# Optimization experiments

Measured on AMD Instinct MI355X. Metric: run time of the kernel, lower is better.

## Reference

```python
import jax, jax.numpy as jnp
import numpy as np

HIDDEN = 2048
HEADS = 32
GROUPS = 8
HEAD_DIM = HIDDEN // HEADS  # 64
BSZ = 1
SEQ = 2048
KV_DIM = GROUPS * HEAD_DIM  # 512


def setup_inputs() -> dict:
    key = jax.random.key(0)
    ks = jax.random.split(key, 10)
    scale = 1.0 / np.sqrt(HIDDEN)
    x = jax.random.normal(ks[0], (BSZ, SEQ, HIDDEN), dtype=jnp.float32)
    # causal mask: 1 where attention is disallowed (strictly upper triangular)
    causal_mask = jnp.triu(jnp.ones((SEQ, SEQ), dtype=jnp.float32), k=1)
    Wq = jax.random.normal(ks[1], (HIDDEN, HIDDEN), dtype=jnp.float32) * scale
    bq = jnp.zeros((HIDDEN,), dtype=jnp.float32)
    Wk = jax.random.normal(ks[2], (HIDDEN, KV_DIM), dtype=jnp.float32) * scale
    bk = jnp.zeros((KV_DIM,), dtype=jnp.float32)
    Wv = jax.random.normal(ks[3], (HIDDEN, KV_DIM), dtype=jnp.float32) * scale
    bv = jnp.zeros((KV_DIM,), dtype=jnp.float32)
    Wo = jax.random.normal(ks[4], (HIDDEN, HIDDEN), dtype=jnp.float32) * scale
    bo = jnp.zeros((HIDDEN,), dtype=jnp.float32)
    return {"x": x, "causal_mask": causal_mask, "Wq": Wq, "bq": bq,
            "Wk": Wk, "bk": bk, "Wv": Wv, "bv": bv, "Wo": Wo, "bo": bo}


def reference(x, causal_mask, Wq, bq, Wk, bk, Wv, bv, Wo, bo):
    b, s, _ = x.shape
    r = HEADS // GROUPS  # queries per KV group
    # projections
    q = (x @ Wq + bq).reshape(b, s, HEADS, HEAD_DIM).transpose(0, 2, 1, 3)   # [b,H,s,d]
    k = (x @ Wk + bk).reshape(b, s, GROUPS, HEAD_DIM).transpose(0, 2, 1, 3)  # [b,G,s,d]
    v = (x @ Wv + bv).reshape(b, s, GROUPS, HEAD_DIM).transpose(0, 2, 1, 3)  # [b,G,s,d]
    # group query heads: head h belongs to group h // r (matches torch expand/reshape order)
    qg = q.reshape(b, GROUPS, r, s, HEAD_DIM)
    inv_sqrt_d = 1.0 / jnp.sqrt(jnp.float32(HEAD_DIM))
    # scores without physically expanding K/V across heads
    scores = jnp.einsum('bgrsd,bgtd->bgrst', qg, k) * inv_sqrt_d  # [b,G,r,s,t]
    scores = scores + causal_mask * (-1e9)
    attn = jax.nn.softmax(scores, axis=-1)
    out = jnp.einsum('bgrst,bgtd->bgrsd', attn, v)                 # [b,G,r,s,d]
    out = out.reshape(b, HEADS, s, HEAD_DIM).transpose(0, 2, 1, 3).reshape(b, s, HIDDEN)
    return out @ Wo + bo
```

## Files before the change

kernel.cpp:

```cpp
#include <hip/hip_runtime.h>

typedef __attribute__((ext_vector_type(8))) short short8;
typedef __attribute__((ext_vector_type(4))) float f32x4;
typedef unsigned short us4 __attribute__((ext_vector_type(4)));
typedef unsigned int u32x2 __attribute__((ext_vector_type(2)));

#define S_LEN 2048
#define HID   2048
#define KVD   512
#define NH    32
#define NG    8
#define HD    64

__device__ __forceinline__ float b2f(ushort u) {
  union { uint i; float f; } c; c.i = ((uint)u) << 16; return c.f;
}
__device__ __forceinline__ ushort f2b(float f) {
  union { float f; uint u; } c; c.f = f;
  uint u = c.u;
  uint r = (u + 0x7FFFu + ((u >> 16) & 1u)) >> 16;
  return (ushort)r;
}

__device__ __forceinline__ void gld_lds16(const ushort* g, short* l) {
  __builtin_amdgcn_global_load_lds(
      (const __attribute__((address_space(1))) void*)g,
      (__attribute__((address_space(3))) void*)l, 16, 0, 0);
}

__global__ __launch_bounds__(256) void detect_dtype(
    const uint* __restrict__ mask, int* __restrict__ flagp)
{
  __shared__ int s_f32;
  if (threadIdx.x == 0) s_f32 = 1;
  __syncthreads();
  int bad = 0;
  for (int i = threadIdx.x; i < 8192; i += 256) {
    const uint w = mask[i];
    if (w != 0u && w != 0x3F800000u) bad = 1;
  }
  if (bad) s_f32 = 0;
  __syncthreads();
  if (threadIdx.x == 0) *flagp = s_f32;
}

__global__ __launch_bounds__(256) void convert_x(
    const void* __restrict__ src, ushort* __restrict__ dst, int n,
    const int* __restrict__ flagp)
{
  const int i = (blockIdx.x * 256 + threadIdx.x) * 4;
  if (i >= n) return;
  if (*flagp) {
    const f32x4 v = *(const f32x4*)((const float*)src + i);
    us4 o;
    o.x = f2b(v.x); o.y = f2b(v.y); o.z = f2b(v.z); o.w = f2b(v.w);
    *(us4*)(dst + i) = o;
  } else {
    *(us4*)(dst + i) = *(const us4*)((const ushort*)src + i);
  }
}

__global__ __launch_bounds__(256) void transpose_any(
    const void* __restrict__ src, ushort* __restrict__ dst, int R, int C,
    const int* __restrict__ flagp)
{
  const int f32 = *flagp;
  __shared__ ushort tile[32][33];
  const int x  = blockIdx.x * 32 + threadIdx.x;
  const int y0 = blockIdx.y * 32;
  for (int i = threadIdx.y; i < 32; i += 8) {
    const size_t idx = (size_t)(y0 + i) * C + x;
    tile[i][threadIdx.x] = f32 ? f2b(((const float*)src)[idx])
                               : ((const ushort*)src)[idx];
  }
  __syncthreads();
  const int xo  = blockIdx.y * 32 + threadIdx.x;
  const int yo0 = blockIdx.x * 32;
  for (int i = threadIdx.y; i < 32; i += 8)
    dst[(size_t)(yo0 + i) * R + xo] = tile[threadIdx.x][i];
}

struct GemmRegions {
  const ushort* Bt[3];
  const void*   bias[3];
  void*         out[3];
  int   ldo[3];
  int   trans[3];
  int   outf32[3];
  float scale[3];
  int   colStart[3];
  int   colEnd[3];
};

__global__ __launch_bounds__(256) void gemm_bt_kernel(
    const ushort* __restrict__ A, int M, int K, GemmRegions rg,
    const int* __restrict__ flagp)
{
  __shared__ __align__(16) short As[128 * 32];
  __shared__ __align__(16) short Bs[128 * 32];

  const int tid  = threadIdx.x;
  const int wave = tid >> 6;
  const int lane = tid & 63;
  const int wm = wave & 1, wn = wave >> 1;
  const int quad = lane >> 4, l16 = lane & 15;

  const int rowBase = blockIdx.y * 128;
  const int colBase = blockIdx.x * 128;

  int ri = 0;
#pragma unroll
  for (int i = 0; i < 3; ++i)
    if (colBase >= rg.colStart[i] && colBase < rg.colEnd[i]) ri = i;

  const int colLocal0   = colBase - rg.colStart[ri];
  const ushort* BtBase  = rg.Bt[ri] + (size_t)colLocal0 * K;
  const void* bias      = rg.bias[ri];
  void* outp            = rg.out[ri];
  const int   ldo   = rg.ldo[ri];
  const int   trans = rg.trans[ri];
  const int   of32  = rg.outf32[ri];
  const float scale = rg.scale[ri];

  const int sRow = tid >> 2;
  const int sCol = (tid & 3) * 8;

  const ushort* a0 = A + (size_t)(rowBase + sRow) * K + sCol;
  const ushort* a1 = A + (size_t)(rowBase + sRow + 64) * K + sCol;
  const ushort* b0 = BtBase + (size_t)sRow * K + sCol;
  const ushort* b1 = BtBase + (size_t)(sRow + 64) * K + sCol;

  const int waveRow = wave * 16;
  short* AsW0 = &As[waveRow * 32];
  short* AsW1 = &As[(waveRow + 64) * 32];
  short* BsW0 = &Bs[waveRow * 32];
  short* BsW1 = &Bs[(waveRow + 64) * 32];

  f32x4 acc[4][4] = {};

  for (int k0 = 0; k0 < K; k0 += 32) {
    __syncthreads();
    gld_lds16(a0 + k0, AsW0);
    gld_lds16(a1 + k0, AsW1);
    gld_lds16(b0 + k0, BsW0);
    gld_lds16(b1 + k0, BsW1);
    __syncthreads();

    short8 af[4], bf[4];
#pragma unroll
    for (int mi = 0; mi < 4; ++mi)
      af[mi] = *(const short8*)&As[(wm * 64 + mi * 16 + l16) * 32 + quad * 8];
#pragma unroll
    for (int ni = 0; ni < 4; ++ni)
      bf[ni] = *(const short8*)&Bs[(wn * 64 + ni * 16 + l16) * 32 + quad * 8];

#pragma unroll
    for (int mi = 0; mi < 4; ++mi)
#pragma unroll
      for (int ni = 0; ni < 4; ++ni)
        acc[mi][ni] = __builtin_amdgcn_mfma_f32_16x16x32_bf16(
            af[mi], bf[ni], acc[mi][ni], 0, 0, 0);
  }

  const int f32io = *flagp;

#pragma unroll
  for (int ni = 0; ni < 4; ++ni) {
    const int cl = wn * 64 + ni * 16 + l16;
    const float bv = f32io ? ((const float*)bias)[colLocal0 + cl]
                           : b2f(((const ushort*)bias)[colLocal0 + cl]);
#pragma unroll
    for (int mi = 0; mi < 4; ++mi) {
      const int row0 = rowBase + wm * 64 + mi * 16 + quad * 4;
#pragma unroll
      for (int r = 0; r < 4; ++r) {
        const float val = (acc[mi][ni][r] + bv) * scale;
        if (!trans) {
          const size_t off = (size_t)(row0 + r) * ldo + colLocal0 + cl;
          if (of32 && f32io) ((float*)outp)[off] = val;
          else               ((ushort*)outp)[off] = f2b(val);
        } else {
          ((ushort*)outp)[(size_t)(colLocal0 + cl) * M + row0 + r] = f2b(val);
        }
      }
    }
  }
}

#define PSTR 40

__global__ __launch_bounds__(256, 2) void attn_kernel(
    const ushort* __restrict__ Q, const ushort* __restrict__ Kb,
    const ushort* __restrict__ Vt, ushort* __restrict__ O)
{
  __shared__ __align__(16) short Pls[4][64 * PSTR];

  const int tid  = threadIdx.x;
  const int wave = tid >> 6;
  const int lane = tid & 63;
  const int quad = lane >> 4, l16 = lane & 15;

  const int h = blockIdx.y;
  const int g = h >> 2;
  const int qbase = blockIdx.x * 256 + wave * 64;

  short8 qfB[4][2];
#pragma unroll
  for (int qf = 0; qf < 4; ++qf) {
    const ushort* qr = Q + (size_t)(qbase + qf * 16 + l16) * HID + h * HD;
#pragma unroll
    for (int ks = 0; ks < 2; ++ks)
      qfB[qf][ks] = *(const short8*)(qr + ks * 32 + quad * 8);
  }

  short8 ones;
#pragma unroll
  for (int j = 0; j < 8; ++j) ones[j] = (short)0x3F80;

  f32x4 o_acc[4][4] = {};
  f32x4 l_acc[4] = {};

  short* pb = &Pls[wave][0];
  const int nfull = qbase >> 5;

  auto body = [&](int it, bool edge) {
    const int t0 = it * 32;

    short8 kA[2][2];
#pragma unroll
    for (int kt = 0; kt < 2; ++kt) {
      const ushort* kr = Kb + (size_t)(t0 + kt * 16 + l16) * KVD + g * HD;
#pragma unroll
      for (int ks = 0; ks < 2; ++ks)
        kA[kt][ks] = *(const short8*)(kr + ks * 32 + quad * 8);
    }

#pragma unroll
    for (int qf = 0; qf < 4; ++qf) {
#pragma unroll
      for (int kt = 0; kt < 2; ++kt) {
        f32x4 z = {};
        z = __builtin_amdgcn_mfma_f32_16x16x32_bf16(kA[kt][0], qfB[qf][0], z, 0, 0, 0);
        z = __builtin_amdgcn_mfma_f32_16x16x32_bf16(kA[kt][1], qfB[qf][1], z, 0, 0, 0);
        ushort p[4];
#pragma unroll
        for (int r = 0; r < 4; ++r) {
          float pv = __expf(z[r]);
          if (edge) {
            const int key = t0 + kt * 16 + quad * 4 + r;
            const int qq  = qbase + qf * 16 + l16;
            if (key > qq) pv = 0.f;
          }
          p[r] = f2b(pv);
        }
        u32x2 w;
        w.x = (uint)p[0] | ((uint)p[1] << 16);
        w.y = (uint)p[2] | ((uint)p[3] << 16);
        *(u32x2*)&pb[(qf * 16 + l16) * PSTR + kt * 16 + quad * 4] = w;
      }
    }

    asm volatile("s_waitcnt lgkmcnt(0)" ::: "memory");

    short8 vB[4];
#pragma unroll
    for (int df = 0; df < 4; ++df)
      vB[df] = *(const short8*)(Vt + (size_t)(g * 64 + df * 16 + l16) * S_LEN
                                + t0 + quad * 8);

#pragma unroll
    for (int qf = 0; qf < 4; ++qf) {
      const short8 pa = *(const short8*)&pb[(qf * 16 + l16) * PSTR + quad * 8];
      l_acc[qf] = __builtin_amdgcn_mfma_f32_16x16x32_bf16(pa, ones, l_acc[qf], 0, 0, 0);
#pragma unroll
      for (int df = 0; df < 4; ++df)
        o_acc[qf][df] = __builtin_amdgcn_mfma_f32_16x16x32_bf16(
            pa, vB[df], o_acc[qf][df], 0, 0, 0);
    }
  };

  for (int it = 0; it < nfull; ++it) body(it, false);
  body(nfull, true);
  body(nfull + 1, true);

#pragma unroll
  for (int qf = 0; qf < 4; ++qf) {
    f32x4 linv;
#pragma unroll
    for (int r = 0; r < 4; ++r) linv[r] = 1.f / l_acc[qf][r];
#pragma unroll
    for (int df = 0; df < 4; ++df)
#pragma unroll
      for (int r = 0; r < 4; ++r)
        O[(size_t)(qbase + qf * 16 + quad * 4 + r) * HID + h * HD + df * 16 + l16]
            = f2b(o_acc[qf][df][r] * linv[r]);
  }
}

extern "C" void kernel_launch(void* const* d_in, const int* in_sizes, int n_in,
                              void* d_out, int out_size, void* d_ws, size_t ws_size,
                              hipStream_t stream) {
  (void)in_sizes; (void)n_in; (void)out_size; (void)ws_size;

  int* flagp = (int*)d_ws;
  ushort* base = (ushort*)d_ws + 16;
  const int M4 = 2048 * 2048;
  const int M1 = 512 * 2048;

  ushort* xb  = base;
  ushort* Wqt = xb  + M4;
  ushort* Wkt = Wqt + M4;
  ushort* Wvt = Wkt + M1;
  ushort* Qb  = Wvt + M1;
  ushort* Kb  = Qb  + M4;
  ushort* Vt  = Kb  + M1;
  ushort* Ob  = Wqt;
  ushort* Wot = Qb;

  detect_dtype<<<1, 256, 0, stream>>>((const uint*)d_in[1], flagp);
  convert_x<<<M4 / 1024, 256, 0, stream>>>(d_in[0], xb, M4, flagp);

  dim3 tb(32, 8);
  transpose_any<<<dim3(64, 64), tb, 0, stream>>>(d_in[2], Wqt, 2048, 2048, flagp);
  transpose_any<<<dim3(16, 64), tb, 0, stream>>>(d_in[4], Wkt, 2048, 512, flagp);
  transpose_any<<<dim3(16, 64), tb, 0, stream>>>(d_in[6], Wvt, 2048, 512, flagp);

  GemmRegions rq;
  rq.Bt[0] = Wqt; rq.bias[0] = d_in[3]; rq.out[0] = Qb; rq.ldo[0] = 2048;
  rq.trans[0] = 0; rq.outf32[0] = 0; rq.scale[0] = 0.125f;
  rq.colStart[0] = 0;    rq.colEnd[0] = 2048;
  rq.Bt[1] = Wkt; rq.bias[1] = d_in[5]; rq.out[1] = Kb; rq.ldo[1] = 512;
  rq.trans[1] = 0; rq.outf32[1] = 0; rq.scale[1] = 1.0f;
  rq.colStart[1] = 2048; rq.colEnd[1] = 2560;
  rq.Bt[2] = Wvt; rq.bias[2] = d_in[7]; rq.out[2] = Vt; rq.ldo[2] = 0;
  rq.trans[2] = 1; rq.outf32[2] = 0; rq.scale[2] = 1.0f;
  rq.colStart[2] = 2560; rq.colEnd[2] = 3072;
  gemm_bt_kernel<<<dim3(3072 / 128, 2048 / 128), 256, 0, stream>>>(
      xb, 2048, 2048, rq, flagp);

  attn_kernel<<<dim3(2048 / 256, NH), 256, 0, stream>>>(Qb, Kb, Vt, Ob);

  transpose_any<<<dim3(64, 64), tb, 0, stream>>>(d_in[8], Wot, 2048, 2048, flagp);

  GemmRegions ro;
  ro.Bt[0] = Wot; ro.bias[0] = d_in[9]; ro.out[0] = d_out; ro.ldo[0] = 2048;
  ro.trans[0] = 0; ro.outf32[0] = 1; ro.scale[0] = 1.0f;
  ro.colStart[0] = 0; ro.colEnd[0] = 2048;
  for (int i = 1; i < 3; ++i) {
    ro.Bt[i] = Wot; ro.bias[i] = d_in[9]; ro.out[i] = d_out; ro.ldo[i] = 2048;
    ro.trans[i] = 0; ro.outf32[i] = 1; ro.scale[i] = 1.0f;
    ro.colStart[i] = 0; ro.colEnd[i] = 0;
  }
  gemm_bt_kernel<<<dim3(2048 / 128, 2048 / 128), 256, 0, stream>>>(
      Ob, 2048, 2048, ro, flagp);
}
```

Measured before the change: 359.8 us.

## Double-buffer K/V register loads in attention loop to prefetch next tile

Restructures the attention inner loop into a two-stage software pipeline: K and V fragments for the next 32-key tile are loaded into a second register set while the current tile's QK, exp and PV MFMAs run. V loads are also issued before the score computation instead of after it. This aims to hide global-memory latency behind compute, at the cost of more live VGPRs and a clamped extra load at the end of the loop.

```diff
diff --git a/kernel.cpp b/kernel.cpp
--- a/kernel.cpp
+++ b/kernel.cpp
@@ -189,6 +189,71 @@
 
 #define PSTR 40
 
+#define MFMA16(A, B, C) __builtin_amdgcn_mfma_f32_16x16x32_bf16(A, B, C, 0, 0, 0)
+
+#define LOADKV(IT, K00, K01, K10, K11, V0, V1, V2, V3)                        \
+  {                                                                           \
+    int t0_ = (IT) * 32;                                                      \
+    if (t0_ > S_LEN - 32) t0_ = S_LEN - 32;                                   \
+    const ushort* kr0_ = Kb + (size_t)(t0_ + l16) * KVD + g * HD + quad * 8;  \
+    const ushort* kr1_ = kr0_ + (size_t)16 * KVD;                             \
+    K00 = *(const short8*)(kr0_);                                             \
+    K01 = *(const short8*)(kr0_ + 32);                                        \
+    K10 = *(const short8*)(kr1_);                                             \
+    K11 = *(const short8*)(kr1_ + 32);                                        \
+    const ushort* vr_ = Vt + (size_t)(g * 64 + l16) * S_LEN + t0_ + quad * 8; \
+    V0 = *(const short8*)(vr_);                                               \
+    V1 = *(const short8*)(vr_ + (size_t)16 * S_LEN);                          \
+    V2 = *(const short8*)(vr_ + (size_t)32 * S_LEN);                          \
+    V3 = *(const short8*)(vr_ + (size_t)48 * S_LEN);                          \
+  }
+
+#define COMPUTE(IT, K00, K01, K10, K11, V0, V1, V2, V3)                       \
+  {                                                                           \
+    const int t0_ = (IT) * 32;                                                \
+    const bool edge_ = (IT) >= nfull;                                         \
+    _Pragma("unroll")                                                         \
+    for (int qf = 0; qf < 4; ++qf) {                                          \
+      f32x4 z0 = {};                                                          \
+      z0 = MFMA16(K00, qfB[qf][0], z0);                                       \
+      z0 = MFMA16(K01, qfB[qf][1], z0);                                       \
+      f32x4 z1 = {};                                                          \
+      z1 = MFMA16(K10, qfB[qf][0], z1);                                       \
+      z1 = MFMA16(K11, qfB[qf][1], z1);                                       \
+      ushort p0[4], p1[4];                                                    \
+      _Pragma("unroll")                                                       \
+      for (int r = 0; r < 4; ++r) {                                           \
+        float pv0 = __expf(z0[r]);                                            \
+        float pv1 = __expf(z1[r]);                                            \
+        if (edge_) {                                                          \
+          const int qq_ = qbase + qf * 16 + l16;                              \
+          if (t0_ + quad * 4 + r > qq_)      pv0 = 0.f;                       \
+          if (t0_ + 16 + quad * 4 + r > qq_) pv1 = 0.f;                       \
+        }                                                                     \
+        p0[r] = f2b(pv0);                                                     \
+        p1[r] = f2b(pv1);                                                     \
+      }                                                                       \
+      u32x2 w0, w1;                                                           \
+      w0.x = (uint)p0[0] | ((uint)p0[1] << 16);                               \
+      w0.y = (uint)p0[2] | ((uint)p0[3] << 16);                               \
+      w1.x = (uint)p1[0] | ((uint)p1[1] << 16);                               \
+      w1.y = (uint)p1[2] | ((uint)p1[3] << 16);                               \
+      *(u32x2*)&pb[(qf * 16 + l16) * PSTR + quad * 4] = w0;                   \
+      *(u32x2*)&pb[(qf * 16 + l16) * PSTR + 16 + quad * 4] = w1;              \
+    }                                                                         \
+    asm volatile("s_waitcnt lgkmcnt(0)" ::: "memory");                        \
+    _Pragma("unroll")                                                         \
+    for (int qf = 0; qf < 4; ++qf) {                                          \
+      const short8 pa =                                                       \
+          *(const short8*)&pb[(qf * 16 + l16) * PSTR + quad * 8];             \
+      l_acc[qf] = MFMA16(pa, ones, l_acc[qf]);                                \
+      o_acc[qf][0] = MFMA16(pa, V0, o_acc[qf][0]);                            \
+      o_acc[qf][1] = MFMA16(pa, V1, o_acc[qf][1]);                            \
+      o_acc[qf][2] = MFMA16(pa, V2, o_acc[qf][2]);                            \
+      o_acc[qf][3] = MFMA16(pa, V3, o_acc[qf][3]);                            \
+    }                                                                         \
+  }
+
 __global__ __launch_bounds__(256, 2) void attn_kernel(
     const ushort* __restrict__ Q, const ushort* __restrict__ Kb,
     const ushort* __restrict__ Vt, ushort* __restrict__ O)
@@ -222,66 +287,18 @@
 
   short* pb = &Pls[wave][0];
   const int nfull = qbase >> 5;
-
-  auto body = [&](int it, bool edge) {
-    const int t0 = it * 32;
-
-    short8 kA[2][2];
-#pragma unroll
-    for (int kt = 0; kt < 2; ++kt) {
-      const ushort* kr = Kb + (size_t)(t0 + kt * 16 + l16) * KVD + g * HD;
-#pragma unroll
-      for (int ks = 0; ks < 2; ++ks)
-        kA[kt][ks] = *(const short8*)(kr + ks * 32 + quad * 8);
-    }
-
-#pragma unroll
-    for (int qf = 0; qf < 4; ++qf) {
-#pragma unroll
-      for (int kt = 0; kt < 2; ++kt) {
-        f32x4 z = {};
-        z = __builtin_amdgcn_mfma_f32_16x16x32_bf16(kA[kt][0], qfB[qf][0], z, 0, 0, 0);
-        z = __builtin_amdgcn_mfma_f32_16x16x32_bf16(kA[kt][1], qfB[qf][1], z, 0, 0, 0);
-        ushort p[4];
-#pragma unroll
-        for (int r = 0; r < 4; ++r) {
-          float pv = __expf(z[r]);
-          if (edge) {
-            const int key = t0 + kt * 16 + quad * 4 + r;
-            const int qq  = qbase + qf * 16 + l16;
-            if (key > qq) pv = 0.f;
-          }
-          p[r] = f2b(pv);
-        }
-        u32x2 w;
-        w.x = (uint)p[0] | ((uint)p[1] << 16);
-        w.y = (uint)p[2] | ((uint)p[3] << 16);
-        *(u32x2*)&pb[(qf * 16 + l16) * PSTR + kt * 16 + quad * 4] = w;
-      }
-    }
-
-    asm volatile("s_waitcnt lgkmcnt(0)" ::: "memory");
-
-    short8 vB[4];
-#pragma unroll
-    for (int df = 0; df < 4; ++df)
-      vB[df] = *(const short8*)(Vt + (size_t)(g * 64 + df * 16 + l16) * S_LEN
-                                + t0 + quad * 8);
-
-#pragma unroll
-    for (int qf = 0; qf < 4; ++qf) {
-      const short8 pa = *(const short8*)&pb[(qf * 16 + l16) * PSTR + quad * 8];
-      l_acc[qf] = __builtin_amdgcn_mfma_f32_16x16x32_bf16(pa, ones, l_acc[qf], 0, 0, 0);
-#pragma unroll
-      for (int df = 0; df < 4; ++df)
-        o_acc[qf][df] = __builtin_amdgcn_mfma_f32_16x16x32_bf16(
-            pa, vB[df], o_acc[qf][df], 0, 0, 0);
-    }
-  };
-
-  for (int it = 0; it < nfull; ++it) body(it, false);
-  body(nfull, true);
-  body(nfull + 1, true);
+  const int total = nfull + 2;
+
+  short8 ka00, ka01, ka10, ka11, va0, va1, va2, va3;
+  short8 kb00, kb01, kb10, kb11, vb0, vb1, vb2, vb3;
+
+  LOADKV(0, ka00, ka01, ka10, ka11, va0, va1, va2, va3);
+  for (int it = 0; it < total; it += 2) {
+    LOADKV(it + 1, kb00, kb01, kb10, kb11, vb0, vb1, vb2, vb3);
+    COMPUTE(it, ka00, ka01, ka10, ka11, va0, va1, va2, va3);
+    LOADKV(it + 2, ka00, ka01, ka10, ka11, va0, va1, va2, va3);
+    COMPUTE(it + 1, kb00, kb01, kb10, kb11, vb0, vb1, vb2, vb3);
+  }
 
 #pragma unroll
   for (int qf = 0; qf < 4; ++qf) {
```

Result: faster. 348.5 us (-3.1%).
